# Optimization experiments

Hardware: AMD Instinct MI355X
Metric: run time of the kernel (lower is better)

The kernel has to match this reference:

```python
import jax, jax.numpy as jnp
import numpy as np

D_MODEL = 1024
H = 16
D_K = D_MODEL // H  # 64
RANK = 5
ALPHA = 1.0


def _lora_linear(x, W, b, dW, dB):
    # merged weight: W + alpha * dB @ dW  (shape [out, in]); F.linear -> x @ W_merged.T + b
    Wm = W + ALPHA * (dB @ dW)
    return x @ Wm.T + b


def setup_inputs() -> dict:
    key = jax.random.key(0)
    ks = jax.random.split(key, 16)
    b_s, nq = 2, 2048
    s = 1.0 / np.sqrt(D_MODEL).astype(np.float32)
    inp = {
        "x": jax.random.normal(ks[0], (b_s, nq, D_MODEL), dtype=jnp.float32),
    }
    names = ["q", "k", "v", "o"]
    i = 1
    for n in names:
        inp[f"{n}_w"] = jax.random.normal(ks[i], (D_MODEL, D_MODEL), dtype=jnp.float32) * s; i += 1
        inp[f"{n}_b"] = jnp.zeros((D_MODEL,), dtype=jnp.float32)
        inp[f"{n}_dw"] = jax.random.normal(ks[i], (RANK, D_MODEL), dtype=jnp.float32) * 0.01; i += 1
        inp[f"{n}_db"] = jax.random.normal(ks[i], (D_MODEL, RANK), dtype=jnp.float32) * 0.01; i += 1
    return inp


def reference(x, q_w, q_b, q_dw, q_db, k_w, k_b, k_dw, k_db,
              v_w, v_b, v_dw, v_db, o_w, o_b, o_dw, o_db):
    b_s, nq, _ = x.shape
    q = _lora_linear(x, q_w, q_b, q_dw, q_db).reshape(b_s, nq, H, D_K)
    k = _lora_linear(x, k_w, k_b, k_dw, k_db).reshape(b_s, nq, H, D_K)
    v = _lora_linear(x, v_w, v_b, v_dw, v_db).reshape(b_s, nq, H, D_K)
    # scores: [b, h, q, k]
    att = jnp.einsum("bqhd,bkhd->bhqk", q, k) / np.sqrt(D_K).astype(np.float32)
    att = jax.nn.softmax(att, axis=-1)
    out = jnp.einsum("bhqk,bkhd->bqhd", att, v).reshape(b_s, nq, H * D_K)
    out = _lora_linear(out, o_w, o_b, o_dw, o_db)
    return out
```

## Files before the change

kernel.cpp:

```cpp
#include <hip/hip_runtime.h>
#include <hip/hip_bf16.h>

#define NQ 2048
#define NB 2

typedef unsigned short u16;
typedef unsigned int u32;
typedef _Float16 f16;
typedef __attribute__((ext_vector_type(8))) _Float16 half8;
typedef __attribute__((ext_vector_type(2))) __fp16 fp16x2;
typedef __attribute__((ext_vector_type(4))) float f32x4;
typedef __attribute__((ext_vector_type(2))) unsigned int u32x2;

#define MFMAH(A, B, C) __builtin_amdgcn_mfma_f32_16x16x32_f16(A, B, C, 0, 0, 0)

__device__ __forceinline__ u16 f2h(float x) {
    f16 h = (f16)x;
    return *(u16*)&h;
}
__device__ __forceinline__ u32 pk_h2(float a, float b) {
    union { fp16x2 v; u32 u; } c;
    c.v = __builtin_amdgcn_cvt_pkrtz(a, b);
    return c.u;
}
__device__ __forceinline__ float fexp2(float x) {
#if __has_builtin(__builtin_amdgcn_exp2f)
    return __builtin_amdgcn_exp2f(x);
#else
    return exp2f(x);
#endif
}
__device__ __forceinline__ void glds16(const u16* g, u16* l) {
    typedef const __attribute__((address_space(1))) u16 gu16;
    typedef __attribute__((address_space(3))) u16 lu16;
    __builtin_amdgcn_global_load_lds((gu16*)g, (lu16*)l, 16, 0, 0);
}
__device__ __forceinline__ void pl32swap(u32& a, u32& b) {
#if __has_builtin(__builtin_amdgcn_permlane32_swap)
    u32x2 r = __builtin_amdgcn_permlane32_swap(a, b, false, false);
    a = r[0]; b = r[1];
#else
    asm volatile("v_permlane32_swap_b32 %0, %1" : "+v"(a), "+v"(b));
#endif
}
__device__ __forceinline__ void pl16swap(u32& a, u32& b) {
#if __has_builtin(__builtin_amdgcn_permlane16_swap)
    u32x2 r = __builtin_amdgcn_permlane16_swap(a, b, false, false);
    a = r[0]; b = r[1];
#else
    asm volatile("v_permlane16_swap_b32 %0, %1" : "+v"(a), "+v"(b));
#endif
}

#define QSCALE 0.18033688011112042f

__global__ __launch_bounds__(256) void merge_w16(
    const float* __restrict__ w0, const float* __restrict__ dw0, const float* __restrict__ db0,
    const float* __restrict__ w1, const float* __restrict__ dw1, const float* __restrict__ db1,
    const float* __restrict__ w2, const float* __restrict__ dw2, const float* __restrict__ db2,
    const float* __restrict__ w3, const float* __restrict__ dw3, const float* __restrict__ db3,
    u16* __restrict__ Wf,
    const float* __restrict__ b0, const float* __restrict__ b1,
    const float* __restrict__ b2, const float* __restrict__ b3,
    float* __restrict__ ball) {
    if (blockIdx.x >= 4096) {
        int t = (blockIdx.x - 4096) * 256 + threadIdx.x;
        int which = t >> 10;
        const float* B = (which == 0) ? b0 : (which == 1) ? b1 : (which == 2) ? b2 : b3;
        float v = B[t & 1023];
        if (which == 0) v *= QSCALE;
        ball[t] = v;
        return;
    }
    int i4 = (blockIdx.x * 256 + threadIdx.x) * 4;
    int row = i4 >> 10, col = i4 & 1023;
    int which = row >> 10, lr = row & 1023;
    const float* W  = (which == 0) ? w0  : (which == 1) ? w1  : (which == 2) ? w2  : w3;
    const float* dW = (which == 0) ? dw0 : (which == 1) ? dw1 : (which == 2) ? dw2 : dw3;
    const float* dB = (which == 0) ? db0 : (which == 1) ? db1 : (which == 2) ? db2 : db3;
    float4 acc = *(const float4*)&W[lr * 1024 + col];
#pragma unroll
    for (int r = 0; r < 5; ++r) {
        float s = dB[lr * 5 + r];
        float4 w4 = *(const float4*)&dW[r * 1024 + col];
        acc.x += s * w4.x; acc.y += s * w4.y;
        acc.z += s * w4.z; acc.w += s * w4.w;
    }
    if (which == 0) { acc.x *= QSCALE; acc.y *= QSCALE; acc.z *= QSCALE; acc.w *= QSCALE; }
    ushort4 o = make_ushort4(f2h(acc.x), f2h(acc.y), f2h(acc.z), f2h(acc.w));
    *(ushort4*)&Wf[i4] = o;
}

__global__ __launch_bounds__(256) void xcast(const float* __restrict__ x,
                                             u16* __restrict__ xf) {
    int i4 = (blockIdx.x * 256 + threadIdx.x) * 4;
    float4 v = *(const float4*)&x[i4];
    *(uint2*)&xf[i4] = make_uint2(pk_h2(v.x, v.y), pk_h2(v.z, v.w));
}

template <int TM>
__global__ __launch_bounds__(256) void gemm_f16(
    const u16* __restrict__ Af, const u16* __restrict__ Bf,
    const float* __restrict__ bias,
    float* __restrict__ Cf, u16* __restrict__ Cb, int ldc,
    u16* __restrict__ VtOut) {
    constexpr int MI = TM / 32;
    __shared__ u16 As[2][TM * 32];
    __shared__ u16 Bs[2][128 * 32];
    const int tid = threadIdx.x;
    const int wid = tid >> 6, lane = tid & 63;
    const int ln = lane & 15, quad = lane >> 4;
    const int bm = blockIdx.y * TM, bn = blockIdx.x * 128;
    const int wm = (wid >> 1) * (TM / 2), wn = (wid & 1) * 64;
    const int lrow = lane >> 2;
    const int schunk = ((lane & 3) ^ ((lrow >> 1) & 3)) * 8;
    const int kswz = (quad ^ ((ln >> 1) & 3)) * 8;

    f32x4 acc[MI][4];
#pragma unroll
    for (int i = 0; i < MI; ++i)
#pragma unroll
        for (int j = 0; j < 4; ++j) acc[i][j] = (f32x4){0.f, 0.f, 0.f, 0.f};

    auto GSTAGE = [&](int k0, int bu) {
#pragma unroll
        for (int p = 0; p < TM / 64; ++p) {
            int r = p * 64 + wid * 16;
            glds16(&Af[(bm + r + lrow) * 1024 + k0 + schunk], &As[bu][r * 32]);
        }
#pragma unroll
        for (int p = 0; p < 2; ++p) {
            int r = p * 64 + wid * 16;
            glds16(&Bf[(bn + r + lrow) * 1024 + k0 + schunk], &Bs[bu][r * 32]);
        }
    };

    auto COMPUTE = [&](int cur) {
        half8 a[MI], b[4];
#pragma unroll
        for (int j = 0; j < 4; ++j)
            b[j] = *(const half8*)&Bs[cur][(wn + j * 16 + ln) * 32 + kswz];
#pragma unroll
        for (int i = 0; i < MI; ++i)
            a[i] = *(const half8*)&As[cur][(wm + i * 16 + ln) * 32 + kswz];
#pragma unroll
        for (int i = 0; i < MI; ++i)
#pragma unroll
            for (int j = 0; j < 4; ++j)
                acc[i][j] = MFMAH(a[i], b[j], acc[i][j]);
    };

    GSTAGE(0, 0);
    asm volatile("s_waitcnt vmcnt(0)" ::: "memory");
    __syncthreads();

    for (int k0 = 0; k0 < 1024 - 32; k0 += 32) {
        const int cur = (k0 >> 5) & 1;
        GSTAGE(k0 + 32, cur ^ 1);
        COMPUTE(cur);
        asm volatile("s_waitcnt vmcnt(0)" ::: "memory");
        __syncthreads();
    }
    COMPUTE(1);

    if (VtOut && bn >= 2048) {
#pragma unroll
        for (int i = 0; i < MI; ++i)
#pragma unroll
            for (int j = 0; j < 4; ++j) {
                int col = bn + wn + j * 16 + ln;
                float bv = bias[col];
                int colV = col - 2048;
                int row0 = bm + wm + i * 16 + quad * 4;
                ushort4 pk = make_ushort4(f2h(acc[i][j][0] + bv), f2h(acc[i][j][1] + bv),
                                          f2h(acc[i][j][2] + bv), f2h(acc[i][j][3] + bv));
                *(ushort4*)&VtOut[colV * 4096 + row0] = pk;
            }
        return;
    }

#pragma unroll
    for (int i = 0; i < MI; ++i)
#pragma unroll
        for (int j = 0; j < 4; ++j) {
            int col = bn + wn + j * 16 + ln;
            float bv = bias[col];
#pragma unroll
            for (int r = 0; r < 4; ++r) {
                int row = bm + wm + i * 16 + quad * 4 + r;
                float v = acc[i][j][r] + bv;
                if (Cb) Cb[row * ldc + col] = f2h(v);
                else    Cf[row * ldc + col] = v;
            }
        }
}

__global__ __launch_bounds__(256) void flash_f16(
    const u16* __restrict__ QKV, const u16* __restrict__ Vt,
    u16* __restrict__ AO) {
    __shared__ u16 Ks[2][2][64 * 32];
    __shared__ u16 Vs[2][2][64 * 32];

    const int tid = threadIdx.x;
    const int wid = tid >> 6, lane = tid & 63;
    const int ln = lane & 15, quad = lane >> 4;
    const int qt = blockIdx.x, h = blockIdx.y, b = blockIdx.z;
    const int rowbase = b * NQ;
    const int col0 = h * 64;
    const int q0 = rowbase + qt * 128 + wid * 32;
    const int lrow = lane >> 2;
    const int kchunk = ((lane & 3) ^ ((lrow >> 1) & 3)) * 8;
    const int kswz = (quad ^ ((ln >> 1) & 3)) * 8;

    const half8 ones = {(f16)1, (f16)1, (f16)1, (f16)1,
                        (f16)1, (f16)1, (f16)1, (f16)1};

    half8 qf[2][2];
#pragma unroll
    for (int mi = 0; mi < 2; ++mi)
#pragma unroll
        for (int kc = 0; kc < 2; ++kc)
            qf[mi][kc] = *(const half8*)&QKV[(q0 + mi * 16 + ln) * 3072 + col0 +
                                             kc * 32 + quad * 8];

    f32x4 accO[4][2];
    f32x4 accS[2];
#pragma unroll
    for (int mi = 0; mi < 2; ++mi) {
        accS[mi] = (f32x4){0.f, 0.f, 0.f, 0.f};
#pragma unroll
        for (int a = 0; a < 4; ++a) accO[a][mi] = (f32x4){0.f, 0.f, 0.f, 0.f};
    }

    const int NT = NQ / 64;
    const u16* Kg = QKV + (rowbase + wid * 16 + lrow) * 3072 + 1024 + col0 + kchunk;
    const u16* Vg = Vt + (col0 + wid * 16 + lrow) * 4096 + rowbase + kchunk;

#define STAGEK(kt2, bu)                                        \
    {                                                          \
        const u16* kg_ = Kg + (kt2) * (64 * 3072);             \
        glds16(kg_,      &Ks[bu][0][wid * 512]);               \
        glds16(kg_ + 32, &Ks[bu][1][wid * 512]);               \
    }
#define STAGEV(kt2, bu)                                        \
    {                                                          \
        const u16* vg_ = Vg + (kt2) * 64;                      \
        glds16(vg_,      &Vs[bu][0][wid * 512]);               \
        glds16(vg_ + 32, &Vs[bu][1][wid * 512]);               \
    }

    auto qk_exp = [&](int kb, half8 (&pf)[2][2]) {
        f32x4 s[4][2];
#pragma unroll
        for (int a = 0; a < 4; ++a) {
            half8 kf0 = *(const half8*)&Ks[kb][0][(a * 16 + ln) * 32 + kswz];
            half8 kf1 = *(const half8*)&Ks[kb][1][(a * 16 + ln) * 32 + kswz];
#pragma unroll
            for (int mi = 0; mi < 2; ++mi) {
                f32x4 t = (f32x4){0.f, 0.f, 0.f, 0.f};
                t = MFMAH(kf0, qf[mi][0], t);
                t = MFMAH(kf1, qf[mi][1], t);
                s[a][mi] = t;
            }
        }
#pragma unroll
        for (int mi = 0; mi < 2; ++mi)
#pragma unroll
            for (int kc = 0; kc < 2; ++kc) {
                u32 c0 = pk_h2(fexp2(s[2 * kc][mi][0]), fexp2(s[2 * kc][mi][1]));
                u32 c1 = pk_h2(fexp2(s[2 * kc][mi][2]), fexp2(s[2 * kc][mi][3]));
                u32 c2 = pk_h2(fexp2(s[2 * kc + 1][mi][0]), fexp2(s[2 * kc + 1][mi][1]));
                u32 c3 = pk_h2(fexp2(s[2 * kc + 1][mi][2]), fexp2(s[2 * kc + 1][mi][3]));
                pl32swap(c0, c2);
                pl32swap(c1, c3);
                pl16swap(c0, c2);
                pl16swap(c1, c3);
                union { u32 u[4]; half8 h; } pu;
                pu.u[0] = c0; pu.u[1] = c1; pu.u[2] = c2; pu.u[3] = c3;
                pf[mi][kc] = pu.h;
                accS[mi] = MFMAH(ones, pf[mi][kc], accS[mi]);
            }
    };

    auto pv = [&](const half8 (&pf)[2][2], int vb) {
#pragma unroll
        for (int a = 0; a < 4; ++a) {
            half8 vf0 = *(const half8*)&Vs[vb][0][(a * 16 + ln) * 32 + kswz];
            half8 vf1 = *(const half8*)&Vs[vb][1][(a * 16 + ln) * 32 + kswz];
#pragma unroll
            for (int mi = 0; mi < 2; ++mi) {
                accO[a][mi] = MFMAH(vf0, pf[mi][0], accO[a][mi]);
                accO[a][mi] = MFMAH(vf1, pf[mi][1], accO[a][mi]);
            }
        }
    };

    half8 pfA[2][2], pfB[2][2];

    STAGEK(0, 0);
    STAGEV(0, 0);
    asm volatile("s_waitcnt vmcnt(0)" ::: "memory");
    __syncthreads();
    STAGEK(1, 1);
    qk_exp(0, pfA);
    asm volatile("s_waitcnt vmcnt(0)" ::: "memory");
    __syncthreads();

    for (int kt = 0; kt < NT - 2; kt += 2) {
        STAGEK(kt + 2, 0);
        STAGEV(kt + 1, 1);
        qk_exp(1, pfB);
        pv(pfA, 0);
        asm volatile("s_waitcnt vmcnt(0)" ::: "memory");
        __syncthreads();

        STAGEK(kt + 3, 1);
        STAGEV(kt + 2, 0);
        qk_exp(0, pfA);
        pv(pfB, 1);
        asm volatile("s_waitcnt vmcnt(0)" ::: "memory");
        __syncthreads();
    }
    STAGEV(NT - 1, 1);
    qk_exp(1, pfB);
    pv(pfA, 0);
    asm volatile("s_waitcnt vmcnt(0)" ::: "memory");
    __syncthreads();
    pv(pfB, 1);
#undef STAGEK
#undef STAGEV

#pragma unroll
    for (int mi = 0; mi < 2; ++mi) {
        float inv = 1.f / accS[mi][0];
        int q = q0 + mi * 16 + ln;
#pragma unroll
        for (int a = 0; a < 4; ++a) {
            ushort4 pk = make_ushort4(f2h(accO[a][mi][0] * inv),
                                      f2h(accO[a][mi][1] * inv),
                                      f2h(accO[a][mi][2] * inv),
                                      f2h(accO[a][mi][3] * inv));
            *(ushort4*)&AO[q * 1024 + col0 + a * 16 + quad * 4] = pk;
        }
    }
}

extern "C" void kernel_launch(void* const* d_in, const int* in_sizes, int n_in,
                              void* d_out, int out_size, void* d_ws, size_t ws_size,
                              hipStream_t stream) {
    const float* x = (const float*)d_in[0];
    const float* w[4]  = {(const float*)d_in[1],  (const float*)d_in[5],
                          (const float*)d_in[9],  (const float*)d_in[13]};
    const float* bv[4] = {(const float*)d_in[2],  (const float*)d_in[6],
                          (const float*)d_in[10], (const float*)d_in[14]};
    const float* dw[4] = {(const float*)d_in[3],  (const float*)d_in[7],
                          (const float*)d_in[11], (const float*)d_in[15]};
    const float* db[4] = {(const float*)d_in[4],  (const float*)d_in[8],
                          (const float*)d_in[12], (const float*)d_in[16]};

    u16* p = (u16*)d_ws;
    u16* Wf  = p; p += 4096 * 1024;
    u16* xf  = p; p += 4096 * 1024;
    u16* QKV = p; p += 4096 * 3072;
    u16* Vt  = p; p += 1024 * 4096;
    float* ball = (float*)p;
    u16* AO = xf;

    merge_w16<<<4112, 256, 0, stream>>>(w[0], dw[0], db[0], w[1], dw[1], db[1],
                                        w[2], dw[2], db[2], w[3], dw[3], db[3], Wf,
                                        bv[0], bv[1], bv[2], bv[3], ball);
    xcast<<<4096, 256, 0, stream>>>(x, xf);

    gemm_f16<128><<<dim3(24, 32), 256, 0, stream>>>(xf, Wf, ball,
                                                    nullptr, QKV, 3072, Vt);

    flash_f16<<<dim3(NQ / 128, 16, NB), 256, 0, stream>>>(QKV, Vt, AO);

    gemm_f16<64><<<dim3(8, 64), 256, 0, stream>>>(AO, Wf + 3072 * 1024,
                                                  ball + 3072, (float*)d_out, nullptr, 1024,
                                                  nullptr);
}
```

Baseline: 225.2 us.

## Triple-buffer GEMM LDS staging and fuse weight-merge with x cast kernel

The GEMM moves from a double-buffered K loop with a full vmcnt(0) drain each step to a three-stage LDS ring. Each step keeps one stage of global-to-LDS loads in flight while computing on the current buffer, waiting only for the older stage via a partial vmcnt. Separately, the weight-merge and x-cast kernels are folded into one launch to save a kernel launch and its gap. The ring raises LDS use by half, which may cut occupancy, and depends on exact vmcnt counts matching the loads issued per stage.

```diff
diff --git a/kernel.cpp b/kernel.cpp
--- a/kernel.cpp
+++ b/kernel.cpp
@@ -35,6 +35,12 @@
     typedef __attribute__((address_space(3))) u16 lu16;
     __builtin_amdgcn_global_load_lds((gu16*)g, (lu16*)l, 16, 0, 0);
 }
+template <int N> __device__ __forceinline__ void waitvm() {
+    if constexpr (N == 0) asm volatile("s_waitcnt vmcnt(0)" ::: "memory");
+    else if constexpr (N == 3) asm volatile("s_waitcnt vmcnt(3)" ::: "memory");
+    else if constexpr (N == 4) asm volatile("s_waitcnt vmcnt(4)" ::: "memory");
+    else static_assert(N == 0 || N == 3 || N == 4, "add vmcnt case");
+}
 __device__ __forceinline__ void pl32swap(u32& a, u32& b) {
 #if __has_builtin(__builtin_amdgcn_permlane32_swap)
     u32x2 r = __builtin_amdgcn_permlane32_swap(a, b, false, false);
@@ -54,17 +60,19 @@
 
 #define QSCALE 0.18033688011112042f
 
-__global__ __launch_bounds__(256) void merge_w16(
+__global__ __launch_bounds__(256) void prep(
     const float* __restrict__ w0, const float* __restrict__ dw0, const float* __restrict__ db0,
     const float* __restrict__ w1, const float* __restrict__ dw1, const float* __restrict__ db1,
     const float* __restrict__ w2, const float* __restrict__ dw2, const float* __restrict__ db2,
     const float* __restrict__ w3, const float* __restrict__ dw3, const float* __restrict__ db3,
     u16* __restrict__ Wf,
+    const float* __restrict__ x, u16* __restrict__ xf,
     const float* __restrict__ b0, const float* __restrict__ b1,
     const float* __restrict__ b2, const float* __restrict__ b3,
     float* __restrict__ ball) {
-    if (blockIdx.x >= 4096) {
-        int t = (blockIdx.x - 4096) * 256 + threadIdx.x;
+    const int bid = blockIdx.x;
+    if (bid >= 8192) {
+        int t = (bid - 8192) * 256 + threadIdx.x;
         int which = t >> 10;
         const float* B = (which == 0) ? b0 : (which == 1) ? b1 : (which == 2) ? b2 : b3;
         float v = B[t & 1023];
@@ -72,7 +80,13 @@
         ball[t] = v;
         return;
     }
-    int i4 = (blockIdx.x * 256 + threadIdx.x) * 4;
+    if (bid >= 4096) {
+        int i4 = ((bid - 4096) * 256 + threadIdx.x) * 4;
+        float4 v = *(const float4*)&x[i4];
+        *(uint2*)&xf[i4] = make_uint2(pk_h2(v.x, v.y), pk_h2(v.z, v.w));
+        return;
+    }
+    int i4 = (bid * 256 + threadIdx.x) * 4;
     int row = i4 >> 10, col = i4 & 1023;
     int which = row >> 10, lr = row & 1023;
     const float* W  = (which == 0) ? w0  : (which == 1) ? w1  : (which == 2) ? w2  : w3;
@@ -89,13 +103,6 @@
     if (which == 0) { acc.x *= QSCALE; acc.y *= QSCALE; acc.z *= QSCALE; acc.w *= QSCALE; }
     ushort4 o = make_ushort4(f2h(acc.x), f2h(acc.y), f2h(acc.z), f2h(acc.w));
     *(ushort4*)&Wf[i4] = o;
-}
-
-__global__ __launch_bounds__(256) void xcast(const float* __restrict__ x,
-                                             u16* __restrict__ xf) {
-    int i4 = (blockIdx.x * 256 + threadIdx.x) * 4;
-    float4 v = *(const float4*)&x[i4];
-    *(uint2*)&xf[i4] = make_uint2(pk_h2(v.x, v.y), pk_h2(v.z, v.w));
 }
 
 template <int TM>
@@ -105,8 +112,9 @@
     float* __restrict__ Cf, u16* __restrict__ Cb, int ldc,
     u16* __restrict__ VtOut) {
     constexpr int MI = TM / 32;
-    __shared__ u16 As[2][TM * 32];
-    __shared__ u16 Bs[2][128 * 32];
+    constexpr int LPS = TM / 64 + 2;
+    __shared__ u16 As[3][TM * 32];
+    __shared__ u16 Bs[3][128 * 32];
     const int tid = threadIdx.x;
     const int wid = tid >> 6, lane = tid & 63;
     const int ln = lane & 15, quad = lane >> 4;
@@ -122,27 +130,27 @@
 #pragma unroll
         for (int j = 0; j < 4; ++j) acc[i][j] = (f32x4){0.f, 0.f, 0.f, 0.f};
 
-    auto GSTAGE = [&](int k0, int bu) {
+    auto GSTAGE = [&](int s, int bu) {
 #pragma unroll
         for (int p = 0; p < TM / 64; ++p) {
             int r = p * 64 + wid * 16;
-            glds16(&Af[(bm + r + lrow) * 1024 + k0 + schunk], &As[bu][r * 32]);
+            glds16(&Af[(bm + r + lrow) * 1024 + s * 32 + schunk], &As[bu][r * 32]);
         }
 #pragma unroll
         for (int p = 0; p < 2; ++p) {
             int r = p * 64 + wid * 16;
-            glds16(&Bf[(bn + r + lrow) * 1024 + k0 + schunk], &Bs[bu][r * 32]);
+            glds16(&Bf[(bn + r + lrow) * 1024 + s * 32 + schunk], &Bs[bu][r * 32]);
         }
     };
 
-    auto COMPUTE = [&](int cur) {
+    auto COMPUTE = [&](int bu) {
         half8 a[MI], b[4];
 #pragma unroll
         for (int j = 0; j < 4; ++j)
-            b[j] = *(const half8*)&Bs[cur][(wn + j * 16 + ln) * 32 + kswz];
+            b[j] = *(const half8*)&Bs[bu][(wn + j * 16 + ln) * 32 + kswz];
 #pragma unroll
         for (int i = 0; i < MI; ++i)
-            a[i] = *(const half8*)&As[cur][(wm + i * 16 + ln) * 32 + kswz];
+            a[i] = *(const half8*)&As[bu][(wm + i * 16 + ln) * 32 + kswz];
 #pragma unroll
         for (int i = 0; i < MI; ++i)
 #pragma unroll
@@ -151,16 +159,18 @@
     };
 
     GSTAGE(0, 0);
-    asm volatile("s_waitcnt vmcnt(0)" ::: "memory");
-    __syncthreads();
-
-    for (int k0 = 0; k0 < 1024 - 32; k0 += 32) {
-        const int cur = (k0 >> 5) & 1;
-        GSTAGE(k0 + 32, cur ^ 1);
-        COMPUTE(cur);
-        asm volatile("s_waitcnt vmcnt(0)" ::: "memory");
-        __syncthreads();
-    }
+    GSTAGE(1, 1);
+    waitvm<LPS>();
+    __syncthreads();
+
+    for (int s = 0; s < 30; s += 3) {
+        GSTAGE(s + 2, 2); COMPUTE(0); waitvm<LPS>(); __syncthreads();
+        GSTAGE(s + 3, 0); COMPUTE(1); waitvm<LPS>(); __syncthreads();
+        GSTAGE(s + 4, 1); COMPUTE(2); waitvm<LPS>(); __syncthreads();
+    }
+    COMPUTE(0);
+    waitvm<0>();
+    __syncthreads();
     COMPUTE(1);
 
     if (VtOut && bn >= 2048) {
@@ -366,10 +376,10 @@
     float* ball = (float*)p;
     u16* AO = xf;
 
-    merge_w16<<<4112, 256, 0, stream>>>(w[0], dw[0], db[0], w[1], dw[1], db[1],
-                                        w[2], dw[2], db[2], w[3], dw[3], db[3], Wf,
-                                        bv[0], bv[1], bv[2], bv[3], ball);
-    xcast<<<4096, 256, 0, stream>>>(x, xf);
+    prep<<<8208, 256, 0, stream>>>(w[0], dw[0], db[0], w[1], dw[1], db[1],
+                                   w[2], dw[2], db[2], w[3], dw[3], db[3], Wf,
+                                   x, xf,
+                                   bv[0], bv[1], bv[2], bv[3], ball);
 
     gemm_f16<128><<<dim3(24, 32), 256, 0, stream>>>(xf, Wf, ball,
                                                     nullptr, QKV, 3072, Vt);
```

Result: faster. 217.7 us (-3.3%).
